# Kernel tuning notes

Measured on AMD Instinct MI355X. Metric: run time of the kernel, lower is better.

The kernel has to match this reference:

```python
import jax, jax.numpy as jnp
import numpy as np

BN_EPS = 1e-5


def _sparse(x, idx, W, b):
    # x: [B, N], idx: [N, K] int, W: [N, K], b: [N]
    # out[b, j] = sum_k x[b, idx[j, k]] * W[j, k] + b[j]
    g = jnp.take(x, idx, axis=1)            # [B, N, K]
    return jnp.einsum('bjk,jk->bj', g, W) + b


def _bn_train(x, gamma, beta):
    # BatchNorm1d in training mode: batch stats, biased variance
    m = jnp.mean(x, axis=0)
    v = jnp.mean(jnp.square(x - m), axis=0)
    return gamma * (x - m) * jax.lax.rsqrt(v + BN_EPS) + beta


def setup_inputs() -> dict:
    key = jax.random.key(0)
    ks = jax.random.split(key, 12)
    B, N = 16384, 784
    s = 0.5  # modest weight scale to keep the deep reuse-chain numerically tame
    return {
        'x':    jax.random.normal(ks[0], (B, N), dtype=jnp.float32),
        'idx1': jax.random.randint(ks[1], (N, 2), 0, N, dtype=jnp.int32),
        'W1':   jax.random.normal(ks[2], (N, 2), dtype=jnp.float32) * s,
        'b1':   jax.random.normal(ks[3], (N,), dtype=jnp.float32) * 0.1,
        'idx2': jax.random.randint(ks[4], (N, 4), 0, N, dtype=jnp.int32),
        'W2':   jax.random.normal(ks[5], (N, 4), dtype=jnp.float32) * s,
        'b2':   jax.random.normal(ks[6], (N,), dtype=jnp.float32) * 0.1,
        'idx3': jax.random.randint(ks[7], (N, 8), 0, N, dtype=jnp.int32),
        'W3':   jax.random.normal(ks[8], (N, 8), dtype=jnp.float32) * s,
        'b3':   jax.random.normal(ks[9], (N,), dtype=jnp.float32) * 0.1,
        'g2':   jnp.ones((N,), dtype=jnp.float32),
        'be2':  jnp.zeros((N,), dtype=jnp.float32),
        'g3':   jnp.ones((N,), dtype=jnp.float32),
        'be3':  jnp.zeros((N,), dtype=jnp.float32),
    }


def reference(x, idx1, W1, b1, idx2, W2, b2, idx3, W3, b3, g2, be2, g3, be3):
    gelu = lambda h: jax.nn.gelu(h, approximate=False)  # torch nn.GELU default (exact)
    h = gelu(_sparse(x, idx1, W1, b1))                  # sp1 -> gelu
    h = _bn_train(gelu(_sparse(h, idx2, W2, b2)), g2, be2)   # sp2 -> gelu -> bn2
    h = _bn_train(gelu(_sparse(h, idx3, W3, b3)), g3, be3)   # sp3 -> gelu -> bn3
    h = _bn_train(gelu(_sparse(h, idx2, W2, b2)), g2, be2)   # sp2 (reused) -> gelu -> bn2
    h = jax.nn.relu(_sparse(h, idx1, W1, b1))                # sp1 (reused) -> relu
    return h
```

## Files before the change

kernel.cpp:

```cpp
#include <hip/hip_runtime.h>
#include <math.h>

static constexpr int BROWS   = 16384;
static constexpr int NC      = 784;
static constexpr int TRB     = 16;
static constexpr int THREADS = 512;
static constexpr int NBLK    = BROWS / TRB;
static constexpr int NSLOT   = 2;
static constexpr int NREP    = 4;
static constexpr float EPS   = 1e-5f;
static constexpr float INV_B = 1.0f / (float)BROWS;

#if defined(__has_builtin)
#if __has_builtin(__builtin_amdgcn_global_load_lds)
#define HAVE_ASYNC_LDS 1
#endif
#if __has_builtin(__builtin_amdgcn_rcpf)
#define HAVE_RCPF 1
#endif
#endif

__device__ __forceinline__ void stage16(const float4* g, float4* l) {
#ifdef HAVE_ASYNC_LDS
    __builtin_amdgcn_global_load_lds(
        (const __attribute__((address_space(1))) void*)g,
        (__attribute__((address_space(3))) void*)l, 16, 0, 0);
#else
    *l = *g;
#endif
}

__device__ __forceinline__ unsigned short f2b(float f) {
    union { float f; unsigned u; } v; v.f = f;
    const unsigned r = v.u + 0x7fffu + ((v.u >> 16) & 1u);
    return (unsigned short)(r >> 16);
}
__device__ __forceinline__ unsigned pack2(float lo, float hi) {
    return (unsigned)f2b(lo) | ((unsigned)f2b(hi) << 16);
}
__device__ __forceinline__ unsigned long long pack4(float a, float b, float c, float d) {
    return (unsigned long long)pack2(a, b) | ((unsigned long long)pack2(c, d) << 32);
}
__device__ __forceinline__ void unpack4(unsigned long long v, float f[4]) {
    const unsigned lo = (unsigned)v, hi = (unsigned)(v >> 32);
    union { unsigned u; float f; } a, b, c, d;
    a.u = lo << 16; b.u = lo & 0xffff0000u; c.u = hi << 16; d.u = hi & 0xffff0000u;
    f[0] = a.f; f[1] = b.f; f[2] = c.f; f[3] = d.f;
}

__device__ __forceinline__ float fast_rcp(float x) {
#ifdef HAVE_RCPF
    return __builtin_amdgcn_rcpf(x);
#else
    return 1.0f / x;
#endif
}

__device__ __forceinline__ float gelu_f(float x) {
    const float a = fabsf(x) * 0.7071067811865475f;
    const float t = fast_rcp(fmaf(0.3275911f, a, 1.0f));
    float p = fmaf(t, 1.061405429f, -1.453152027f);
    p = fmaf(t, p, 1.421413741f);
    p = fmaf(t, p, -0.284496736f);
    p = fmaf(t, p, 0.254829592f);
    p *= t;
    const float e  = __expf(-a * a);
    const float er = fmaf(-p, e, 1.0f);
    return 0.5f * x * (1.0f + copysignf(er, x));
}

__global__ __launch_bounds__(THREADS, 8)
void layer12(const float* __restrict__ x,
             const int* __restrict__ idx1, const float* __restrict__ W1, const float* __restrict__ b1,
             const int* __restrict__ idx2, const float* __restrict__ W2, const float* __restrict__ b2,
             unsigned long long* __restrict__ uq2,
             float* __restrict__ ssum, float* __restrict__ ssq)
{
    __shared__ unsigned long long quad[4 * NC];
    const int tid  = threadIdx.x;
    const int row0 = blockIdx.x * TRB;

    #pragma unroll
    for (int slot = 0; slot < NSLOT; ++slot) {
        const int c = tid + slot * THREADS;
        if (c < NC) {
            #pragma unroll
            for (int q = 0; q < 4; ++q) {
                const size_t base = (size_t)(row0 + 4 * q) * NC + c;
                quad[q * NC + c] = pack4(x[base], x[base + NC], x[base + 2 * NC], x[base + 3 * NC]);
            }
        }
    }
    __syncthreads();

    for (int half = 0; half < 2; ++half) {
        float h[NSLOT][8];
        #pragma unroll
        for (int slot = 0; slot < NSLOT; ++slot) {
            const int j = tid + slot * THREADS;
            if (j < NC) {
                const int   i0 = idx1[2 * j], i1 = idx1[2 * j + 1];
                const float w0 = W1[2 * j],   w1 = W1[2 * j + 1], bb = b1[j];
                #pragma unroll
                for (int qq = 0; qq < 2; ++qq) {
                    float f0[4], f1[4];
                    unpack4(quad[(2 * half + qq) * NC + i0], f0);
                    unpack4(quad[(2 * half + qq) * NC + i1], f1);
                    #pragma unroll
                    for (int rr = 0; rr < 4; ++rr)
                        h[slot][4 * qq + rr] = gelu_f(fmaf(f0[rr], w0, fmaf(f1[rr], w1, bb)));
                }
            }
        }
        __syncthreads();
        #pragma unroll
        for (int slot = 0; slot < NSLOT; ++slot) {
            const int j = tid + slot * THREADS;
            if (j < NC) {
                quad[(2 * half + 0) * NC + j] = pack4(h[slot][0], h[slot][1], h[slot][2], h[slot][3]);
                quad[(2 * half + 1) * NC + j] = pack4(h[slot][4], h[slot][5], h[slot][6], h[slot][7]);
            }
        }
        __syncthreads();
    }

    for (int slot = 0; slot < NSLOT; ++slot) {
        const int j = tid + slot * THREADS;
        if (j < NC) {
            int ji[4]; float jw[4];
            #pragma unroll
            for (int k = 0; k < 4; ++k) { ji[k] = idx2[4 * j + k]; jw[k] = W2[4 * j + k]; }
            const float jb = b2[j];
            float s1 = 0.0f, s2 = 0.0f;
            #pragma unroll
            for (int q = 0; q < 4; ++q) {
                float acc[4] = { jb, jb, jb, jb };
                #pragma unroll
                for (int k = 0; k < 4; ++k) {
                    float f[4];
                    unpack4(quad[q * NC + ji[k]], f);
                    #pragma unroll
                    for (int rr = 0; rr < 4; ++rr) acc[rr] = fmaf(f[rr], jw[k], acc[rr]);
                }
                float u[4];
                #pragma unroll
                for (int rr = 0; rr < 4; ++rr) {
                    u[rr] = gelu_f(acc[rr]);
                    s1 += u[rr]; s2 = fmaf(u[rr], u[rr], s2);
                }
                uq2[(size_t)(blockIdx.x * 4 + q) * NC + j] = pack4(u[0], u[1], u[2], u[3]);
            }
            const int rep = blockIdx.x & (NREP - 1);
            atomicAdd(&ssum[rep * NC + j], s1);
            atomicAdd(&ssq[rep * NC + j],  s2);
        }
    }
}

template<int K, bool FINAL>
__global__ __launch_bounds__(THREADS, 8)
void layer_bn(const unsigned long long* __restrict__ uqin,
              const int* __restrict__ idx, const float* __restrict__ W, const float* __restrict__ bias,
              const float* __restrict__ gamma, const float* __restrict__ beta,
              const float* __restrict__ psum, const float* __restrict__ psq,
              unsigned long long* __restrict__ uqout, float* __restrict__ fout,
              float* __restrict__ ssum, float* __restrict__ ssq)
{
    __shared__ unsigned long long quad[4 * NC];
    __shared__ float s_sc[NC], s_sh[NC];
    const int tid  = threadIdx.x;
    const int row0 = blockIdx.x * TRB;

    {
        const float4* src = (const float4*)(uqin + (size_t)blockIdx.x * 4 * NC);
        float4*       dst = (float4*)quad;
        for (int i = tid; i < 4 * NC / 2; i += THREADS) stage16(src + i, dst + i);
    }
    for (int j = tid; j < NC; j += THREADS) {
        float s1 = 0.0f, s2 = 0.0f;
        #pragma unroll
        for (int r = 0; r < NREP; ++r) { s1 += psum[r * NC + j]; s2 += psq[r * NC + j]; }
        const float m   = s1 * INV_B;
        const float var = fmaf(-m, m, s2 * INV_B);
        const float sc  = gamma[j] * rsqrtf(var + EPS);
        s_sc[j] = sc;
        s_sh[j] = fmaf(-m, sc, beta[j]);
    }
    __syncthreads();

    for (int slot = 0; slot < NSLOT; ++slot) {
        const int j = tid + slot * THREADS;
        if (j < NC) {
            int ji[K]; float jw[K];
            float jb = bias[j];
            #pragma unroll
            for (int k = 0; k < K; ++k) {
                const int   c = idx[K * j + k];
                const float w = W[K * j + k];
                ji[k] = c; jw[k] = w * s_sc[c]; jb = fmaf(w, s_sh[c], jb);
            }
            float s1 = 0.0f, s2 = 0.0f;
            #pragma unroll
            for (int q = 0; q < 4; ++q) {
                float acc[4] = { jb, jb, jb, jb };
                #pragma unroll
                for (int k = 0; k < K; ++k) {
                    float f[4];
                    unpack4(quad[q * NC + ji[k]], f);
                    #pragma unroll
                    for (int rr = 0; rr < 4; ++rr) acc[rr] = fmaf(f[rr], jw[k], acc[rr]);
                }
                if (FINAL) {
                    #pragma unroll
                    for (int rr = 0; rr < 4; ++rr)
                        fout[(size_t)(row0 + 4 * q + rr) * NC + j] = fmaxf(acc[rr], 0.0f);
                } else {
                    float u[4];
                    #pragma unroll
                    for (int rr = 0; rr < 4; ++rr) {
                        u[rr] = gelu_f(acc[rr]);
                        s1 += u[rr]; s2 = fmaf(u[rr], u[rr], s2);
                    }
                    uqout[(size_t)(blockIdx.x * 4 + q) * NC + j] = pack4(u[0], u[1], u[2], u[3]);
                }
            }
            if (!FINAL) {
                const int rep = blockIdx.x & (NREP - 1);
                atomicAdd(&ssum[rep * NC + j], s1);
                atomicAdd(&ssq[rep * NC + j],  s2);
            }
        }
    }
}

extern "C" void kernel_launch(void* const* d_in, const int* in_sizes, int n_in,
                              void* d_out, int out_size, void* d_ws, size_t ws_size,
                              hipStream_t stream)
{
    const float* x    = (const float*)d_in[0];
    const int*   idx1 = (const int*)  d_in[1];
    const float* W1   = (const float*)d_in[2];
    const float* b1   = (const float*)d_in[3];
    const int*   idx2 = (const int*)  d_in[4];
    const float* W2   = (const float*)d_in[5];
    const float* b2   = (const float*)d_in[6];
    const int*   idx3 = (const int*)  d_in[7];
    const float* W3   = (const float*)d_in[8];
    const float* b3   = (const float*)d_in[9];
    const float* g2   = (const float*)d_in[10];
    const float* be2  = (const float*)d_in[11];
    const float* g3   = (const float*)d_in[12];
    const float* be3  = (const float*)d_in[13];
    float* out = (float*)d_out;

    const size_t QN = (size_t)NBLK * 4 * NC;
    unsigned long long* ws0 = (unsigned long long*)d_ws;
    unsigned long long* ws1 = ws0 + QN;
    float* p = (float*)(ws1 + QN);
    float* sum2a = p; p += NREP * NC;  float* ssq2a = p; p += NREP * NC;
    float* sum3  = p; p += NREP * NC;  float* ssq3  = p; p += NREP * NC;
    float* sum2b = p; p += NREP * NC;  float* ssq2b = p; p += NREP * NC;

    hipMemsetAsync(sum2a, 0, 6 * NREP * NC * sizeof(float), stream);

    const dim3 grid(NBLK), blk(THREADS);

    layer12<<<grid, blk, 0, stream>>>(x, idx1, W1, b1, idx2, W2, b2, ws0, sum2a, ssq2a);
    layer_bn<8, false><<<grid, blk, 0, stream>>>(
        ws0, idx3, W3, b3, g2, be2, sum2a, ssq2a, ws1, nullptr, sum3, ssq3);
    layer_bn<4, false><<<grid, blk, 0, stream>>>(
        ws1, idx2, W2, b2, g3, be3, sum3, ssq3, ws0, nullptr, sum2b, ssq2b);
    layer_bn<2, true><<<grid, blk, 0, stream>>>(
        ws0, idx1, W1, b1, g2, be2, sum2b, ssq2b, nullptr, out, nullptr, nullptr);
}
```

Baseline: 192.6 us.

## Fuse all layers into a persistent kernel with grid-wide barriers for BN stats

Replaces the four layer launches with one persistent kernel of 1024 blocks. Each block keeps its 16-row activation tile in LDS across all five sparse layers and spin-waits on an atomic grid barrier whenever it needs BatchNorm statistics from the whole batch. This removes the global-memory round trip of packed intermediates between layers, and the launch gaps. It adds barrier spin cost and relies on every block being co-resident: threads drop from 512 to 256, and a residency check picks a multi-kernel fallback otherwise. The check only tests blocks per CU, so the grid can deadlock if not all CUs are available.

```diff
diff --git a/kernel.cpp b/kernel.cpp
--- a/kernel.cpp
+++ b/kernel.cpp
@@ -4,9 +4,9 @@
 static constexpr int BROWS   = 16384;
 static constexpr int NC      = 784;
 static constexpr int TRB     = 16;
-static constexpr int THREADS = 512;
-static constexpr int NBLK    = BROWS / TRB;
-static constexpr int NSLOT   = 2;
+static constexpr int THREADS = 256;
+static constexpr int NTILE   = BROWS / TRB;
+static constexpr int NSLOT   = 4;
 static constexpr int NREP    = 4;
 static constexpr float EPS   = 1e-5f;
 static constexpr float INV_B = 1.0f / (float)BROWS;
@@ -69,17 +69,9 @@
     return 0.5f * x * (1.0f + copysignf(er, x));
 }
 
-__global__ __launch_bounds__(THREADS, 8)
-void layer12(const float* __restrict__ x,
-             const int* __restrict__ idx1, const float* __restrict__ W1, const float* __restrict__ b1,
-             const int* __restrict__ idx2, const float* __restrict__ W2, const float* __restrict__ b2,
-             unsigned long long* __restrict__ uq2,
-             float* __restrict__ ssum, float* __restrict__ ssq)
-{
-    __shared__ unsigned long long quad[4 * NC];
-    const int tid  = threadIdx.x;
-    const int row0 = blockIdx.x * TRB;
-
+__device__ __forceinline__ void stage_x(const float* __restrict__ x,
+                                        unsigned long long* quad, int row0) {
+    const int tid = threadIdx.x;
     #pragma unroll
     for (int slot = 0; slot < NSLOT; ++slot) {
         const int c = tid + slot * THREADS;
@@ -92,94 +84,21 @@
         }
     }
     __syncthreads();
-
-    for (int half = 0; half < 2; ++half) {
-        float h[NSLOT][8];
-        #pragma unroll
-        for (int slot = 0; slot < NSLOT; ++slot) {
-            const int j = tid + slot * THREADS;
-            if (j < NC) {
-                const int   i0 = idx1[2 * j], i1 = idx1[2 * j + 1];
-                const float w0 = W1[2 * j],   w1 = W1[2 * j + 1], bb = b1[j];
-                #pragma unroll
-                for (int qq = 0; qq < 2; ++qq) {
-                    float f0[4], f1[4];
-                    unpack4(quad[(2 * half + qq) * NC + i0], f0);
-                    unpack4(quad[(2 * half + qq) * NC + i1], f1);
-                    #pragma unroll
-                    for (int rr = 0; rr < 4; ++rr)
-                        h[slot][4 * qq + rr] = gelu_f(fmaf(f0[rr], w0, fmaf(f1[rr], w1, bb)));
-                }
-            }
-        }
-        __syncthreads();
-        #pragma unroll
-        for (int slot = 0; slot < NSLOT; ++slot) {
-            const int j = tid + slot * THREADS;
-            if (j < NC) {
-                quad[(2 * half + 0) * NC + j] = pack4(h[slot][0], h[slot][1], h[slot][2], h[slot][3]);
-                quad[(2 * half + 1) * NC + j] = pack4(h[slot][4], h[slot][5], h[slot][6], h[slot][7]);
-            }
-        }
-        __syncthreads();
-    }
-
-    for (int slot = 0; slot < NSLOT; ++slot) {
-        const int j = tid + slot * THREADS;
-        if (j < NC) {
-            int ji[4]; float jw[4];
-            #pragma unroll
-            for (int k = 0; k < 4; ++k) { ji[k] = idx2[4 * j + k]; jw[k] = W2[4 * j + k]; }
-            const float jb = b2[j];
-            float s1 = 0.0f, s2 = 0.0f;
-            #pragma unroll
-            for (int q = 0; q < 4; ++q) {
-                float acc[4] = { jb, jb, jb, jb };
-                #pragma unroll
-                for (int k = 0; k < 4; ++k) {
-                    float f[4];
-                    unpack4(quad[q * NC + ji[k]], f);
-                    #pragma unroll
-                    for (int rr = 0; rr < 4; ++rr) acc[rr] = fmaf(f[rr], jw[k], acc[rr]);
-                }
-                float u[4];
-                #pragma unroll
-                for (int rr = 0; rr < 4; ++rr) {
-                    u[rr] = gelu_f(acc[rr]);
-                    s1 += u[rr]; s2 = fmaf(u[rr], u[rr], s2);
-                }
-                uq2[(size_t)(blockIdx.x * 4 + q) * NC + j] = pack4(u[0], u[1], u[2], u[3]);
-            }
-            const int rep = blockIdx.x & (NREP - 1);
-            atomicAdd(&ssum[rep * NC + j], s1);
-            atomicAdd(&ssq[rep * NC + j],  s2);
-        }
-    }
-}
-
-template<int K, bool FINAL>
-__global__ __launch_bounds__(THREADS, 8)
-void layer_bn(const unsigned long long* __restrict__ uqin,
-              const int* __restrict__ idx, const float* __restrict__ W, const float* __restrict__ bias,
-              const float* __restrict__ gamma, const float* __restrict__ beta,
-              const float* __restrict__ psum, const float* __restrict__ psq,
-              unsigned long long* __restrict__ uqout, float* __restrict__ fout,
-              float* __restrict__ ssum, float* __restrict__ ssq)
-{
-    __shared__ unsigned long long quad[4 * NC];
-    __shared__ float s_sc[NC], s_sh[NC];
-    const int tid  = threadIdx.x;
-    const int row0 = blockIdx.x * TRB;
-
-    {
-        const float4* src = (const float4*)(uqin + (size_t)blockIdx.x * 4 * NC);
-        float4*       dst = (float4*)quad;
-        for (int i = tid; i < 4 * NC / 2; i += THREADS) stage16(src + i, dst + i);
-    }
+}
+
+__device__ __forceinline__ void make_scsh(const float* __restrict__ psum,
+                                          const float* __restrict__ psq,
+                                          const float* __restrict__ gamma,
+                                          const float* __restrict__ beta,
+                                          float* s_sc, float* s_sh) {
+    const int tid = threadIdx.x;
     for (int j = tid; j < NC; j += THREADS) {
         float s1 = 0.0f, s2 = 0.0f;
         #pragma unroll
-        for (int r = 0; r < NREP; ++r) { s1 += psum[r * NC + j]; s2 += psq[r * NC + j]; }
+        for (int r = 0; r < NREP; ++r) {
+            s1 += __hip_atomic_load(&psum[r * NC + j], __ATOMIC_RELAXED, __HIP_MEMORY_SCOPE_AGENT);
+            s2 += __hip_atomic_load(&psq[r * NC + j],  __ATOMIC_RELAXED, __HIP_MEMORY_SCOPE_AGENT);
+        }
         const float m   = s1 * INV_B;
         const float var = fmaf(-m, m, s2 * INV_B);
         const float sc  = gamma[j] * rsqrtf(var + EPS);
@@ -187,49 +106,203 @@
         s_sh[j] = fmaf(-m, sc, beta[j]);
     }
     __syncthreads();
-
+}
+
+template<int K, bool FOLD, bool STATS>
+__device__ __forceinline__ void do_layer(unsigned long long* quad,
+                                         const float* s_sc, const float* s_sh,
+                                         const int* __restrict__ idx,
+                                         const float* __restrict__ W,
+                                         const float* __restrict__ bias,
+                                         float* __restrict__ ssum,
+                                         float* __restrict__ ssq, int rep) {
+    const int tid = threadIdx.x;
+    float st1[NSLOT], st2[NSLOT];
+    if (STATS)
+        #pragma unroll
+        for (int s = 0; s < NSLOT; ++s) { st1[s] = 0.0f; st2[s] = 0.0f; }
+
+    for (int half = 0; half < 2; ++half) {
+        float outv[NSLOT][8];
+        #pragma unroll
+        for (int slot = 0; slot < NSLOT; ++slot) {
+            const int j = tid + slot * THREADS;
+            if (j < NC) {
+                int ji[K]; float jw[K];
+                float jb = bias[j];
+                #pragma unroll
+                for (int k = 0; k < K; ++k) {
+                    const int   c = idx[j * K + k];
+                    const float w = W[j * K + k];
+                    ji[k] = c;
+                    if (FOLD) { jw[k] = w * s_sc[c]; jb = fmaf(w, s_sh[c], jb); }
+                    else        jw[k] = w;
+                }
+                float acc[8];
+                #pragma unroll
+                for (int r = 0; r < 8; ++r) acc[r] = jb;
+                #pragma unroll
+                for (int k = 0; k < K; ++k) {
+                    #pragma unroll
+                    for (int qq = 0; qq < 2; ++qq) {
+                        float f[4];
+                        unpack4(quad[(2 * half + qq) * NC + ji[k]], f);
+                        #pragma unroll
+                        for (int rr = 0; rr < 4; ++rr)
+                            acc[qq * 4 + rr] = fmaf(f[rr], jw[k], acc[qq * 4 + rr]);
+                    }
+                }
+                #pragma unroll
+                for (int r = 0; r < 8; ++r) {
+                    const float u = gelu_f(acc[r]);
+                    outv[slot][r] = u;
+                    if (STATS) { st1[slot] += u; st2[slot] = fmaf(u, u, st2[slot]); }
+                }
+            }
+        }
+        __syncthreads();
+        #pragma unroll
+        for (int slot = 0; slot < NSLOT; ++slot) {
+            const int j = tid + slot * THREADS;
+            if (j < NC) {
+                quad[(2 * half + 0) * NC + j] = pack4(outv[slot][0], outv[slot][1], outv[slot][2], outv[slot][3]);
+                quad[(2 * half + 1) * NC + j] = pack4(outv[slot][4], outv[slot][5], outv[slot][6], outv[slot][7]);
+            }
+        }
+        __syncthreads();
+    }
+    if (STATS) {
+        #pragma unroll
+        for (int slot = 0; slot < NSLOT; ++slot) {
+            const int j = tid + slot * THREADS;
+            if (j < NC) {
+                atomicAdd(&ssum[rep * NC + j], st1[slot]);
+                atomicAdd(&ssq[rep * NC + j],  st2[slot]);
+            }
+        }
+    }
+}
+
+__device__ __forceinline__ void do_final(const unsigned long long* quad,
+                                         const float* s_sc, const float* s_sh,
+                                         const int* __restrict__ idx,
+                                         const float* __restrict__ W,
+                                         const float* __restrict__ bias,
+                                         float* __restrict__ out, int row0) {
+    const int tid = threadIdx.x;
+    #pragma unroll
     for (int slot = 0; slot < NSLOT; ++slot) {
         const int j = tid + slot * THREADS;
         if (j < NC) {
-            int ji[K]; float jw[K];
-            float jb = bias[j];
-            #pragma unroll
-            for (int k = 0; k < K; ++k) {
-                const int   c = idx[K * j + k];
-                const float w = W[K * j + k];
-                ji[k] = c; jw[k] = w * s_sc[c]; jb = fmaf(w, s_sh[c], jb);
-            }
-            float s1 = 0.0f, s2 = 0.0f;
+            const int   c0 = idx[2 * j], c1 = idx[2 * j + 1];
+            const float w0 = W[2 * j],   w1 = W[2 * j + 1];
+            const float jw0 = w0 * s_sc[c0], jw1 = w1 * s_sc[c1];
+            const float jb  = fmaf(w0, s_sh[c0], fmaf(w1, s_sh[c1], bias[j]));
             #pragma unroll
             for (int q = 0; q < 4; ++q) {
-                float acc[4] = { jb, jb, jb, jb };
-                #pragma unroll
-                for (int k = 0; k < K; ++k) {
-                    float f[4];
-                    unpack4(quad[q * NC + ji[k]], f);
-                    #pragma unroll
-                    for (int rr = 0; rr < 4; ++rr) acc[rr] = fmaf(f[rr], jw[k], acc[rr]);
+                float f0[4], f1[4];
+                unpack4(quad[q * NC + c0], f0);
+                unpack4(quad[q * NC + c1], f1);
+                #pragma unroll
+                for (int rr = 0; rr < 4; ++rr) {
+                    const float acc = fmaf(f0[rr], jw0, fmaf(f1[rr], jw1, jb));
+                    out[(size_t)(row0 + 4 * q + rr) * NC + j] = fmaxf(acc, 0.0f);
                 }
-                if (FINAL) {
-                    #pragma unroll
-                    for (int rr = 0; rr < 4; ++rr)
-                        fout[(size_t)(row0 + 4 * q + rr) * NC + j] = fmaxf(acc[rr], 0.0f);
-                } else {
-                    float u[4];
-                    #pragma unroll
-                    for (int rr = 0; rr < 4; ++rr) {
-                        u[rr] = gelu_f(acc[rr]);
-                        s1 += u[rr]; s2 = fmaf(u[rr], u[rr], s2);
-                    }
-                    uqout[(size_t)(blockIdx.x * 4 + q) * NC + j] = pack4(u[0], u[1], u[2], u[3]);
-                }
-            }
-            if (!FINAL) {
-                const int rep = blockIdx.x & (NREP - 1);
-                atomicAdd(&ssum[rep * NC + j], s1);
-                atomicAdd(&ssq[rep * NC + j],  s2);
-            }
-        }
+            }
+        }
+    }
+}
+
+__device__ __forceinline__ void grid_barrier(unsigned* cnt, unsigned* gen, unsigned target) {
+    __syncthreads();
+    if (threadIdx.x == 0) {
+        __threadfence();
+        const unsigned old = __hip_atomic_fetch_add(cnt, 1u, __ATOMIC_ACQ_REL, __HIP_MEMORY_SCOPE_AGENT);
+        if (old == (unsigned)NTILE - 1u) {
+            __hip_atomic_fetch_add(gen, 1u, __ATOMIC_RELEASE, __HIP_MEMORY_SCOPE_AGENT);
+        } else {
+            while (__hip_atomic_load(gen, __ATOMIC_ACQUIRE, __HIP_MEMORY_SCOPE_AGENT) < target)
+                __builtin_amdgcn_s_sleep(2);
+        }
+        __threadfence();
+    }
+    __syncthreads();
+}
+
+__global__ __launch_bounds__(THREADS, 4)
+void persist(const float* __restrict__ x,
+             const int* __restrict__ idx1, const float* __restrict__ W1, const float* __restrict__ b1,
+             const int* __restrict__ idx2, const float* __restrict__ W2, const float* __restrict__ b2,
+             const int* __restrict__ idx3, const float* __restrict__ W3, const float* __restrict__ b3,
+             const float* __restrict__ g2, const float* __restrict__ be2,
+             const float* __restrict__ g3, const float* __restrict__ be3,
+             float* __restrict__ out,
+             float* __restrict__ sum2a, float* __restrict__ ssq2a,
+             float* __restrict__ sum3,  float* __restrict__ ssq3,
+             float* __restrict__ sum2b, float* __restrict__ ssq2b,
+             unsigned* __restrict__ bar)
+{
+    __shared__ __align__(16) unsigned long long quad[4 * NC];
+    __shared__ float s_sc[NC], s_sh[NC];
+    const int row0 = blockIdx.x * TRB;
+    const int rep  = blockIdx.x & (NREP - 1);
+
+    stage_x(x, quad, row0);
+    do_layer<2, false, false>(quad, s_sc, s_sh, idx1, W1, b1, nullptr, nullptr, rep);
+    do_layer<4, false, true >(quad, s_sc, s_sh, idx2, W2, b2, sum2a, ssq2a, rep);
+    grid_barrier(bar + 0, bar + 3, 1u);
+    make_scsh(sum2a, ssq2a, g2, be2, s_sc, s_sh);
+    do_layer<8, true,  true >(quad, s_sc, s_sh, idx3, W3, b3, sum3, ssq3, rep);
+    grid_barrier(bar + 1, bar + 3, 2u);
+    make_scsh(sum3, ssq3, g3, be3, s_sc, s_sh);
+    do_layer<4, true,  true >(quad, s_sc, s_sh, idx2, W2, b2, sum2b, ssq2b, rep);
+    grid_barrier(bar + 2, bar + 3, 3u);
+    make_scsh(sum2b, ssq2b, g2, be2, s_sc, s_sh);
+    do_final(quad, s_sc, s_sh, idx1, W1, b1, out, row0);
+}
+
+__global__ __launch_bounds__(THREADS, 4)
+void fb_layer12(const float* __restrict__ x,
+                const int* __restrict__ idx1, const float* __restrict__ W1, const float* __restrict__ b1,
+                const int* __restrict__ idx2, const float* __restrict__ W2, const float* __restrict__ b2,
+                unsigned long long* __restrict__ uqout,
+                float* __restrict__ ssum, float* __restrict__ ssq)
+{
+    __shared__ __align__(16) unsigned long long quad[4 * NC];
+    const int row0 = blockIdx.x * TRB;
+    const int rep  = blockIdx.x & (NREP - 1);
+    stage_x(x, quad, row0);
+    do_layer<2, false, false>(quad, nullptr, nullptr, idx1, W1, b1, nullptr, nullptr, rep);
+    do_layer<4, false, true >(quad, nullptr, nullptr, idx2, W2, b2, ssum, ssq, rep);
+    for (int i = threadIdx.x; i < 4 * NC; i += THREADS)
+        uqout[(size_t)blockIdx.x * 4 * NC + i] = quad[i];
+}
+
+template<int K, bool FINAL>
+__global__ __launch_bounds__(THREADS, 4)
+void fb_layer_bn(const unsigned long long* __restrict__ uqin,
+                 const int* __restrict__ idx, const float* __restrict__ W, const float* __restrict__ bias,
+                 const float* __restrict__ gamma, const float* __restrict__ beta,
+                 const float* __restrict__ psum, const float* __restrict__ psq,
+                 unsigned long long* __restrict__ uqout, float* __restrict__ fout,
+                 float* __restrict__ ssum, float* __restrict__ ssq)
+{
+    __shared__ __align__(16) unsigned long long quad[4 * NC];
+    __shared__ float s_sc[NC], s_sh[NC];
+    const int row0 = blockIdx.x * TRB;
+    const int rep  = blockIdx.x & (NREP - 1);
+    {
+        const float4* src = (const float4*)(uqin + (size_t)blockIdx.x * 4 * NC);
+        float4*       dst = (float4*)quad;
+        for (int i = threadIdx.x; i < 4 * NC / 2; i += THREADS) stage16(src + i, dst + i);
+    }
+    make_scsh(psum, psq, gamma, beta, s_sc, s_sh);
+    if (FINAL) {
+        do_final(quad, s_sc, s_sh, idx, W, bias, fout, row0);
+    } else {
+        do_layer<K, true, true>(quad, s_sc, s_sh, idx, W, bias, ssum, ssq, rep);
+        for (int i = threadIdx.x; i < 4 * NC; i += THREADS)
+            uqout[(size_t)blockIdx.x * 4 * NC + i] = quad[i];
     }
 }
 
@@ -253,23 +326,35 @@
     const float* be3  = (const float*)d_in[13];
     float* out = (float*)d_out;
 
-    const size_t QN = (size_t)NBLK * 4 * NC;
+    const size_t QN = (size_t)NTILE * 4 * NC;
     unsigned long long* ws0 = (unsigned long long*)d_ws;
     unsigned long long* ws1 = ws0 + QN;
     float* p = (float*)(ws1 + QN);
     float* sum2a = p; p += NREP * NC;  float* ssq2a = p; p += NREP * NC;
     float* sum3  = p; p += NREP * NC;  float* ssq3  = p; p += NREP * NC;
     float* sum2b = p; p += NREP * NC;  float* ssq2b = p; p += NREP * NC;
-
-    hipMemsetAsync(sum2a, 0, 6 * NREP * NC * sizeof(float), stream);
-
-    const dim3 grid(NBLK), blk(THREADS);
-
-    layer12<<<grid, blk, 0, stream>>>(x, idx1, W1, b1, idx2, W2, b2, ws0, sum2a, ssq2a);
-    layer_bn<8, false><<<grid, blk, 0, stream>>>(
-        ws0, idx3, W3, b3, g2, be2, sum2a, ssq2a, ws1, nullptr, sum3, ssq3);
-    layer_bn<4, false><<<grid, blk, 0, stream>>>(
-        ws1, idx2, W2, b2, g3, be3, sum3, ssq3, ws0, nullptr, sum2b, ssq2b);
-    layer_bn<2, true><<<grid, blk, 0, stream>>>(
-        ws0, idx1, W1, b1, g2, be2, sum2b, ssq2b, nullptr, out, nullptr, nullptr);
-}
+    unsigned* bar = (unsigned*)p;
+
+    hipMemsetAsync(sum2a, 0, 6 * NREP * NC * sizeof(float) + 4 * sizeof(unsigned), stream);
+
+    int maxBlk = 0;
+    const hipError_t qerr =
+        hipOccupancyMaxActiveBlocksPerMultiprocessor(&maxBlk, (const void*)persist, THREADS, 0);
+    const bool resident = (qerr == hipSuccess && maxBlk >= 4);
+
+    if (resident) {
+        persist<<<dim3(NTILE), dim3(THREADS), 0, stream>>>(
+            x, idx1, W1, b1, idx2, W2, b2, idx3, W3, b3,
+            g2, be2, g3, be3, out,
+            sum2a, ssq2a, sum3, ssq3, sum2b, ssq2b, bar);
+    } else {
+        const dim3 grid(NTILE), blk(THREADS);
+        fb_layer12<<<grid, blk, 0, stream>>>(x, idx1, W1, b1, idx2, W2, b2, ws0, sum2a, ssq2a);
+        fb_layer_bn<8, false><<<grid, blk, 0, stream>>>(
+            ws0, idx3, W3, b3, g2, be2, sum2a, ssq2a, ws1, nullptr, sum3, ssq3);
+        fb_layer_bn<4, false><<<grid, blk, 0, stream>>>(
+            ws1, idx2, W2, b2, g3, be3, sum3, ssq3, ws0, nullptr, sum2b, ssq2b);
+        fb_layer_bn<2, true><<<grid, blk, 0, stream>>>(
+            ws0, idx1, W1, b1, g2, be2, sum2b, ssq2b, nullptr, out, nullptr, nullptr);
+    }
+}
```

New measurement: 210.8 us. 1.09x slower.

## Pack eight bf16 rows per uint4 with padded LDS stride and register staging

Applied to the files above, without the earlier changes.

Changes the intermediate layout from 4-row bf16 quads (8 bytes) to 8-row bf16 octets (16 bytes), stored per column in a padded LDS tile with a stride of 3 uint4 to reduce bank conflicts. Each gather then fetches 8 rows with one 128-bit LDS read instead of two 64-bit reads. The async global-to-LDS staging is replaced by register loads issued before the BN-stat computation, so the load latency overlaps that work. Occupancy hints drop from 8 to 6 because the larger LDS tile and more live registers would otherwise not fit.

```diff
diff --git a/kernel.cpp b/kernel.cpp
--- a/kernel.cpp
+++ b/kernel.cpp
@@ -6,30 +6,18 @@
 static constexpr int TRB     = 16;
 static constexpr int THREADS = 512;
 static constexpr int NBLK    = BROWS / TRB;
-static constexpr int NSLOT   = 2;
+static constexpr int CHUNK   = 2;
+static constexpr int REGN    = NC * CHUNK;
 static constexpr int NREP    = 4;
 static constexpr float EPS   = 1e-5f;
 static constexpr float INV_B = 1.0f / (float)BROWS;
 
 #if defined(__has_builtin)
-#if __has_builtin(__builtin_amdgcn_global_load_lds)
-#define HAVE_ASYNC_LDS 1
-#endif
 #if __has_builtin(__builtin_amdgcn_rcpf)
 #define HAVE_RCPF 1
 #endif
 #endif
 
-__device__ __forceinline__ void stage16(const float4* g, float4* l) {
-#ifdef HAVE_ASYNC_LDS
-    __builtin_amdgcn_global_load_lds(
-        (const __attribute__((address_space(1))) void*)g,
-        (__attribute__((address_space(3))) void*)l, 16, 0, 0);
-#else
-    *l = *g;
-#endif
-}
-
 __device__ __forceinline__ unsigned short f2b(float f) {
     union { float f; unsigned u; } v; v.f = f;
     const unsigned r = v.u + 0x7fffu + ((v.u >> 16) & 1u);
@@ -38,16 +26,6 @@
 __device__ __forceinline__ unsigned pack2(float lo, float hi) {
     return (unsigned)f2b(lo) | ((unsigned)f2b(hi) << 16);
 }
-__device__ __forceinline__ unsigned long long pack4(float a, float b, float c, float d) {
-    return (unsigned long long)pack2(a, b) | ((unsigned long long)pack2(c, d) << 32);
-}
-__device__ __forceinline__ void unpack4(unsigned long long v, float f[4]) {
-    const unsigned lo = (unsigned)v, hi = (unsigned)(v >> 32);
-    union { unsigned u; float f; } a, b, c, d;
-    a.u = lo << 16; b.u = lo & 0xffff0000u; c.u = hi << 16; d.u = hi & 0xffff0000u;
-    f[0] = a.f; f[1] = b.f; f[2] = c.f; f[3] = d.f;
-}
-
 __device__ __forceinline__ float fast_rcp(float x) {
 #ifdef HAVE_RCPF
     return __builtin_amdgcn_rcpf(x);
@@ -55,7 +33,6 @@
     return 1.0f / x;
 #endif
 }
-
 __device__ __forceinline__ float gelu_f(float x) {
     const float a = fabsf(x) * 0.7071067811865475f;
     const float t = fast_rcp(fmaf(0.3275911f, a, 1.0f));
@@ -69,112 +46,136 @@
     return 0.5f * x * (1.0f + copysignf(er, x));
 }
 
-__global__ __launch_bounds__(THREADS, 8)
-void layer12(const float* __restrict__ x,
-             const int* __restrict__ idx1, const float* __restrict__ W1, const float* __restrict__ b1,
-             const int* __restrict__ idx2, const float* __restrict__ W2, const float* __restrict__ b2,
-             unsigned long long* __restrict__ uq2,
-             float* __restrict__ ssum, float* __restrict__ ssq)
+
+__device__ __forceinline__ void fma8(const uint4 v, const float w, float acc[8]) {
+    const unsigned* u = &v.x;
+    #pragma unroll
+    for (int q = 0; q < 4; ++q) {
+        union { unsigned u; float f; } lo, hi;
+        lo.u = u[q] << 16;
+        hi.u = u[q] & 0xffff0000u;
+        acc[2 * q]     = fmaf(lo.f, w, acc[2 * q]);
+        acc[2 * q + 1] = fmaf(hi.f, w, acc[2 * q + 1]);
+    }
+}
+
+__global__ __launch_bounds__(THREADS, 6)
+void k12(const float* __restrict__ x,
+         const int* __restrict__ idx1, const float* __restrict__ W1, const float* __restrict__ b1,
+         const int* __restrict__ idx2, const float* __restrict__ W2, const float* __restrict__ b2,
+         uint4* __restrict__ outr, float* __restrict__ ssum, float* __restrict__ ssq)
 {
-    __shared__ unsigned long long quad[4 * NC];
+    __shared__ uint4 tile[NC * 3];
     const int tid  = threadIdx.x;
     const int row0 = blockIdx.x * TRB;
 
-    #pragma unroll
-    for (int slot = 0; slot < NSLOT; ++slot) {
-        const int c = tid + slot * THREADS;
-        if (c < NC) {
+    for (int c = tid; c < NC; c += THREADS) {
+        float xr[TRB];
+        #pragma unroll
+        for (int r = 0; r < TRB; ++r) xr[r] = x[(size_t)(row0 + r) * NC + c];
+        #pragma unroll
+        for (int h = 0; h < 2; ++h) {
+            uint4 v;
+            v.x = pack2(xr[8 * h + 0], xr[8 * h + 1]);
+            v.y = pack2(xr[8 * h + 2], xr[8 * h + 3]);
+            v.z = pack2(xr[8 * h + 4], xr[8 * h + 5]);
+            v.w = pack2(xr[8 * h + 6], xr[8 * h + 7]);
+            tile[3 * c + h] = v;
+        }
+    }
+    __syncthreads();
+
+    unsigned hp0[2][4], hp1[2][4];
+    const int j1 = tid + THREADS;
+    const bool act1 = (j1 < NC);
+    {
+        const int   c0 = idx1[2 * tid], c1 = idx1[2 * tid + 1];
+        const float w0 = W1[2 * tid],   w1 = W1[2 * tid + 1], bb = b1[tid];
+        #pragma unroll
+        for (int h = 0; h < 2; ++h) {
+            float acc[8];
+            #pragma unroll
+            for (int r = 0; r < 8; ++r) acc[r] = bb;
+            fma8(tile[3 * c0 + h], w0, acc);
+            fma8(tile[3 * c1 + h], w1, acc);
+            #pragma unroll
+            for (int q = 0; q < 4; ++q)
+                hp0[h][q] = pack2(gelu_f(acc[2 * q]), gelu_f(acc[2 * q + 1]));
+        }
+    }
+    if (act1) {
+        const int   c0 = idx1[2 * j1], c1 = idx1[2 * j1 + 1];
+        const float w0 = W1[2 * j1],   w1 = W1[2 * j1 + 1], bb = b1[j1];
+        #pragma unroll
+        for (int h = 0; h < 2; ++h) {
+            float acc[8];
+            #pragma unroll
+            for (int r = 0; r < 8; ++r) acc[r] = bb;
+            fma8(tile[3 * c0 + h], w0, acc);
+            fma8(tile[3 * c1 + h], w1, acc);
+            #pragma unroll
+            for (int q = 0; q < 4; ++q)
+                hp1[h][q] = pack2(gelu_f(acc[2 * q]), gelu_f(acc[2 * q + 1]));
+        }
+    }
+    __syncthreads();
+    #pragma unroll
+    for (int h = 0; h < 2; ++h) {
+        tile[3 * tid + h] = make_uint4(hp0[h][0], hp0[h][1], hp0[h][2], hp0[h][3]);
+        if (act1)
+            tile[3 * j1 + h] = make_uint4(hp1[h][0], hp1[h][1], hp1[h][2], hp1[h][3]);
+    }
+    __syncthreads();
+
+    const int rep = blockIdx.x & (NREP - 1);
+    uint4* dst = outr + (size_t)blockIdx.x * REGN;
+    for (int j = tid; j < NC; j += THREADS) {
+        int ji[4]; float jw[4];
+        #pragma unroll
+        for (int k = 0; k < 4; ++k) { ji[k] = idx2[4 * j + k]; jw[k] = W2[4 * j + k]; }
+        const float jb = b2[j];
+        float s1 = 0.0f, s2 = 0.0f;
+        #pragma unroll
+        for (int h = 0; h < 2; ++h) {
+            float acc[8];
+            #pragma unroll
+            for (int r = 0; r < 8; ++r) acc[r] = jb;
+            #pragma unroll
+            for (int k = 0; k < 4; ++k) fma8(tile[3 * ji[k] + h], jw[k], acc);
+            unsigned up[4];
             #pragma unroll
             for (int q = 0; q < 4; ++q) {
-                const size_t base = (size_t)(row0 + 4 * q) * NC + c;
-                quad[q * NC + c] = pack4(x[base], x[base + NC], x[base + 2 * NC], x[base + 3 * NC]);
+                const float ulo = gelu_f(acc[2 * q]), uhi = gelu_f(acc[2 * q + 1]);
+                s1 += ulo + uhi; s2 = fmaf(ulo, ulo, fmaf(uhi, uhi, s2));
+                up[q] = pack2(ulo, uhi);
             }
-        }
-    }
-    __syncthreads();
-
-    for (int half = 0; half < 2; ++half) {
-        float h[NSLOT][8];
-        #pragma unroll
-        for (int slot = 0; slot < NSLOT; ++slot) {
-            const int j = tid + slot * THREADS;
-            if (j < NC) {
-                const int   i0 = idx1[2 * j], i1 = idx1[2 * j + 1];
-                const float w0 = W1[2 * j],   w1 = W1[2 * j + 1], bb = b1[j];
-                #pragma unroll
-                for (int qq = 0; qq < 2; ++qq) {
-                    float f0[4], f1[4];
-                    unpack4(quad[(2 * half + qq) * NC + i0], f0);
-                    unpack4(quad[(2 * half + qq) * NC + i1], f1);
-                    #pragma unroll
-                    for (int rr = 0; rr < 4; ++rr)
-                        h[slot][4 * qq + rr] = gelu_f(fmaf(f0[rr], w0, fmaf(f1[rr], w1, bb)));
-                }
-            }
-        }
-        __syncthreads();
-        #pragma unroll
-        for (int slot = 0; slot < NSLOT; ++slot) {
-            const int j = tid + slot * THREADS;
-            if (j < NC) {
-                quad[(2 * half + 0) * NC + j] = pack4(h[slot][0], h[slot][1], h[slot][2], h[slot][3]);
-                quad[(2 * half + 1) * NC + j] = pack4(h[slot][4], h[slot][5], h[slot][6], h[slot][7]);
-            }
-        }
-        __syncthreads();
-    }
-
-    for (int slot = 0; slot < NSLOT; ++slot) {
-        const int j = tid + slot * THREADS;
-        if (j < NC) {
-            int ji[4]; float jw[4];
-            #pragma unroll
-            for (int k = 0; k < 4; ++k) { ji[k] = idx2[4 * j + k]; jw[k] = W2[4 * j + k]; }
-            const float jb = b2[j];
-            float s1 = 0.0f, s2 = 0.0f;
-            #pragma unroll
-            for (int q = 0; q < 4; ++q) {
-                float acc[4] = { jb, jb, jb, jb };
-                #pragma unroll
-                for (int k = 0; k < 4; ++k) {
-                    float f[4];
-                    unpack4(quad[q * NC + ji[k]], f);
-                    #pragma unroll
-                    for (int rr = 0; rr < 4; ++rr) acc[rr] = fmaf(f[rr], jw[k], acc[rr]);
-                }
-                float u[4];
-                #pragma unroll
-                for (int rr = 0; rr < 4; ++rr) {
-                    u[rr] = gelu_f(acc[rr]);
-                    s1 += u[rr]; s2 = fmaf(u[rr], u[rr], s2);
-                }
-                uq2[(size_t)(blockIdx.x * 4 + q) * NC + j] = pack4(u[0], u[1], u[2], u[3]);
-            }
-            const int rep = blockIdx.x & (NREP - 1);
-            atomicAdd(&ssum[rep * NC + j], s1);
-            atomicAdd(&ssq[rep * NC + j],  s2);
-        }
+            dst[2 * j + h] = make_uint4(up[0], up[1], up[2], up[3]);
+        }
+        atomicAdd(&ssum[rep * NC + j], s1);
+        atomicAdd(&ssq[rep * NC + j],  s2);
     }
 }
 
 template<int K, bool FINAL>
-__global__ __launch_bounds__(THREADS, 8)
-void layer_bn(const unsigned long long* __restrict__ uqin,
-              const int* __restrict__ idx, const float* __restrict__ W, const float* __restrict__ bias,
-              const float* __restrict__ gamma, const float* __restrict__ beta,
-              const float* __restrict__ psum, const float* __restrict__ psq,
-              unsigned long long* __restrict__ uqout, float* __restrict__ fout,
-              float* __restrict__ ssum, float* __restrict__ ssq)
+__global__ __launch_bounds__(THREADS, 6)
+void kbn(const uint4* __restrict__ inr,
+         const int* __restrict__ idx, const float* __restrict__ W, const float* __restrict__ bias,
+         const float* __restrict__ gamma, const float* __restrict__ beta,
+         const float* __restrict__ psum, const float* __restrict__ psq,
+         uint4* __restrict__ outr, float* __restrict__ fout,
+         float* __restrict__ ssum, float* __restrict__ ssq)
 {
-    __shared__ unsigned long long quad[4 * NC];
+    __shared__ uint4 tile[NC * 3];
     __shared__ float s_sc[NC], s_sh[NC];
     const int tid  = threadIdx.x;
     const int row0 = blockIdx.x * TRB;
 
-    {
-        const float4* src = (const float4*)(uqin + (size_t)blockIdx.x * 4 * NC);
-        float4*       dst = (float4*)quad;
-        for (int i = tid; i < 4 * NC / 2; i += THREADS) stage16(src + i, dst + i);
+    const uint4* src = inr + (size_t)blockIdx.x * REGN;
+    uint4 sv[4];
+    #pragma unroll
+    for (int t = 0; t < 4; ++t) {
+        const int e = tid + t * THREADS;
+        if (e < REGN) sv[t] = src[e];
     }
     for (int j = tid; j < NC; j += THREADS) {
         float s1 = 0.0f, s2 = 0.0f;
@@ -186,49 +187,50 @@
         s_sc[j] = sc;
         s_sh[j] = fmaf(-m, sc, beta[j]);
     }
-    __syncthreads();
-
-    for (int slot = 0; slot < NSLOT; ++slot) {
-        const int j = tid + slot * THREADS;
-        if (j < NC) {
-            int ji[K]; float jw[K];
-            float jb = bias[j];
-            #pragma unroll
-            for (int k = 0; k < K; ++k) {
-                const int   c = idx[K * j + k];
-                const float w = W[K * j + k];
-                ji[k] = c; jw[k] = w * s_sc[c]; jb = fmaf(w, s_sh[c], jb);
+    #pragma unroll
+    for (int t = 0; t < 4; ++t) {
+        const int e = tid + t * THREADS;
+        if (e < REGN) tile[3 * (e >> 1) + (e & 1)] = sv[t];
+    }
+    __syncthreads();
+
+    const int rep = blockIdx.x & (NREP - 1);
+    uint4* dst = FINAL ? nullptr : (outr + (size_t)blockIdx.x * REGN);
+    for (int j = tid; j < NC; j += THREADS) {
+        int ji[K]; float jw[K];
+        float jb = bias[j];
+        #pragma unroll
+        for (int k = 0; k < K; ++k) {
+            const int   c = idx[K * j + k];
+            const float w = W[K * j + k];
+            ji[k] = c; jw[k] = w * s_sc[c]; jb = fmaf(w, s_sh[c], jb);
+        }
+        float s1 = 0.0f, s2 = 0.0f;
+        #pragma unroll
+        for (int h = 0; h < 2; ++h) {
+            float acc[8];
+            #pragma unroll
+            for (int r = 0; r < 8; ++r) acc[r] = jb;
+            #pragma unroll
+            for (int k = 0; k < K; ++k) fma8(tile[3 * ji[k] + h], jw[k], acc);
+            if (FINAL) {
+                #pragma unroll
+                for (int r = 0; r < 8; ++r)
+                    fout[(size_t)(row0 + 8 * h + r) * NC + j] = fmaxf(acc[r], 0.0f);
+            } else {
+                unsigned up[4];
+                #pragma unroll
+                for (int q = 0; q < 4; ++q) {
+                    const float ulo = gelu_f(acc[2 * q]), uhi = gelu_f(acc[2 * q + 1]);
+                    s1 += ulo + uhi; s2 = fmaf(ulo, ulo, fmaf(uhi, uhi, s2));
+                    up[q] = pack2(ulo, uhi);
+                }
+                dst[2 * j + h] = make_uint4(up[0], up[1], up[2], up[3]);
             }
-            float s1 = 0.0f, s2 = 0.0f;
-            #pragma unroll
-            for (int q = 0; q < 4; ++q) {
-                float acc[4] = { jb, jb, jb, jb };
-                #pragma unroll
-                for (int k = 0; k < K; ++k) {
-                    float f[4];
-                    unpack4(quad[q * NC + ji[k]], f);
-                    #pragma unroll
-                    for (int rr = 0; rr < 4; ++rr) acc[rr] = fmaf(f[rr], jw[k], acc[rr]);
-                }
-                if (FINAL) {
-                    #pragma unroll
-                    for (int rr = 0; rr < 4; ++rr)
-                        fout[(size_t)(row0 + 4 * q + rr) * NC + j] = fmaxf(acc[rr], 0.0f);
-                } else {
-                    float u[4];
-                    #pragma unroll
-                    for (int rr = 0; rr < 4; ++rr) {
-                        u[rr] = gelu_f(acc[rr]);
-                        s1 += u[rr]; s2 = fmaf(u[rr], u[rr], s2);
-                    }
-                    uqout[(size_t)(blockIdx.x * 4 + q) * NC + j] = pack4(u[0], u[1], u[2], u[3]);
-                }
-            }
-            if (!FINAL) {
-                const int rep = blockIdx.x & (NREP - 1);
-                atomicAdd(&ssum[rep * NC + j], s1);
-                atomicAdd(&ssq[rep * NC + j],  s2);
-            }
+        }
+        if (!FINAL) {
+            atomicAdd(&ssum[rep * NC + j], s1);
+            atomicAdd(&ssq[rep * NC + j],  s2);
         }
     }
 }
@@ -253,10 +255,9 @@
     const float* be3  = (const float*)d_in[13];
     float* out = (float*)d_out;
 
-    const size_t QN = (size_t)NBLK * 4 * NC;
-    unsigned long long* ws0 = (unsigned long long*)d_ws;
-    unsigned long long* ws1 = ws0 + QN;
-    float* p = (float*)(ws1 + QN);
+    uint4* r0 = (uint4*)d_ws;
+    uint4* r1 = r0 + (size_t)NBLK * REGN;
+    float* p  = (float*)(r1 + (size_t)NBLK * REGN);
     float* sum2a = p; p += NREP * NC;  float* ssq2a = p; p += NREP * NC;
     float* sum3  = p; p += NREP * NC;  float* ssq3  = p; p += NREP * NC;
     float* sum2b = p; p += NREP * NC;  float* ssq2b = p; p += NREP * NC;
@@ -265,11 +266,11 @@
 
     const dim3 grid(NBLK), blk(THREADS);
 
-    layer12<<<grid, blk, 0, stream>>>(x, idx1, W1, b1, idx2, W2, b2, ws0, sum2a, ssq2a);
-    layer_bn<8, false><<<grid, blk, 0, stream>>>(
-        ws0, idx3, W3, b3, g2, be2, sum2a, ssq2a, ws1, nullptr, sum3, ssq3);
-    layer_bn<4, false><<<grid, blk, 0, stream>>>(
-        ws1, idx2, W2, b2, g3, be3, sum3, ssq3, ws0, nullptr, sum2b, ssq2b);
-    layer_bn<2, true><<<grid, blk, 0, stream>>>(
-        ws0, idx1, W1, b1, g2, be2, sum2b, ssq2b, nullptr, out, nullptr, nullptr);
-}
+    k12<<<grid, blk, 0, stream>>>(x, idx1, W1, b1, idx2, W2, b2, r0, sum2a, ssq2a);
+    kbn<8, false><<<grid, blk, 0, stream>>>(
+        r0, idx3, W3, b3, g2, be2, sum2a, ssq2a, r1, nullptr, sum3, ssq3);
+    kbn<4, false><<<grid, blk, 0, stream>>>(
+        r1, idx2, W2, b2, g3, be3, sum3, ssq3, r0, nullptr, sum2b, ssq2b);
+    kbn<2, true><<<grid, blk, 0, stream>>>(
+        r0, idx1, W1, b1, g2, be2, sum2b, ssq2b, nullptr, out, nullptr, nullptr);
+}
```

Result: slower. 213.8 us (+11.0%).
